# Kernel optimization log

Hardware: AMD Instinct MI355X
Metric: run time of the kernel (lower is better)

The kernel has to match this reference:

```python
import jax, jax.numpy as jnp
import numpy as np
from itertools import combinations

H_RANK_MAX = 2
TP_RANK_MAX = 2
BASIS_RANK_MAX = 2
DIM = 3
N_NODES = 50000
N_EDGES = 400000
N_CHANNELS = 16
R_CUT = 10.0  # radial cutoff for Bessel RBF (assumed)


def find_combinations(a_max, b_max, s):
    if s > a_max + b_max or s < 0:
        return []
    return [(a, s - a) for a in range(max(0, s - b_max), min(a_max, s) + 1)]


def contraction_is_valid(n_in, n_out):
    # legs are removed in pairs (Kronecker-delta contractions)
    return (n_in >= n_out) and ((n_in - n_out) % 2 == 0)


def _matchings(legs):
    # all perfect matchings of an even-size list of leg indices
    if not legs:
        yield []
        return
    a = legs[0]
    for i in range(1, len(legs)):
        rest = legs[1:i] + legs[i + 1:]
        for m in _matchings(rest):
            yield [(a, legs[i])] + m


def contraction_specs(a, b, c_out):
    # all einsum strings contracting an [E,K,dim^a] x [E,K,dim^b] tensor product
    # (a+b legs total) down to c_out free Cartesian legs, pairing the rest.
    n = a + b
    specs = []
    for free in combinations(range(n), c_out):
        paired = [i for i in range(n) if i not in free]
        for m in _matchings(paired):
            lbl = {}
            it = iter('mnopqrstuvwxyz')
            for f in free:
                lbl[f] = next(it)
            for (i, j) in m:
                L = next(it)
                lbl[i] = L
                lbl[j] = L
            sa = ''.join(lbl[i] for i in range(a))
            sb = ''.join(lbl[i] for i in range(a, n))
            so = ''.join(lbl[f] for f in free)
            specs.append(f'ek{sa},ek{sb}->ek{so}')
    return specs


def e_rbf(r, n):
    # Bessel radial basis: n is [K,1], r is [E] -> [K,E]
    return jnp.sqrt(2.0 / R_CUT) * jnp.sin(n * jnp.pi * r / R_CUT) / r


def tensor_prod(r, order):
    # repeated outer product of unit vectors: order 0 -> [E], order k -> [E] + [DIM]*k
    out = jnp.ones(r.shape[0], dtype=r.dtype)
    for _ in range(order):
        out = jnp.einsum('e...,ed->e...d', out, r)
    return out


def setup_inputs() -> dict:
    key = jax.random.key(0)
    ks = jax.random.split(key, 7)
    h0 = jax.random.normal(ks[0], (N_NODES, N_CHANNELS), jnp.float32)
    h1 = jax.random.normal(ks[1], (N_NODES, N_CHANNELS, DIM), jnp.float32)
    h2 = jax.random.normal(ks[2], (N_NODES, N_CHANNELS, DIM, DIM), jnp.float32)
    pos = jax.random.normal(ks[3], (N_NODES, DIM), jnp.float32)
    channel_weights = jax.random.normal(ks[4], (H_RANK_MAX + 1, N_CHANNELS, N_CHANNELS), jnp.float32)
    src = jax.random.randint(ks[5], (N_EDGES,), 0, N_NODES, dtype=jnp.int32)
    off = jax.random.randint(ks[6], (N_EDGES,), 1, N_NODES, dtype=jnp.int32)
    dst = (src + off) % N_NODES  # no self-loops -> no zero distances
    edge_index = jnp.stack([src, dst])
    return {"h0": h0, "h1": h1, "h2": h2, "pos": pos,
            "channel_weights": channel_weights, "edge_index": edge_index}


def reference(h0, h1, h2, pos, channel_weights, edge_index):
    h = [h0, h1, h2]
    src, dst = edge_index[0], edge_index[1]
    rel = pos[src] - pos[dst]                       # [E,3]
    dists = jnp.linalg.norm(rel, axis=-1)           # [E]
    unit = rel / dists[:, None]
    hg = [g[dst] for g in h]                        # per-edge gathered features
    # NOTE: the original forward computes channel-mixed self.h with channel_weights
    # but the contraction loop uses the UNMIXED gathered h (h[split[0]]); replicated here,
    # so channel_weights does not affect the output (zero gradient).
    n_vals = jnp.arange(1, N_CHANNELS + 1, dtype=dists.dtype)[:, None]  # [K,1]
    radial = e_rbf(dists, n_vals).reshape(N_EDGES, N_CHANNELS)  # faithful reshape (not transpose), as in source
    r_raw = [tensor_prod(unit, o) for o in range(TP_RANK_MAX + 1)]
    r_w = [jnp.einsum('ek,e...->ek...', radial, t) for t in r_raw]  # [E,K]+[3]*b
    outs = [None] * (BASIS_RANK_MAX + 1)
    for n_ind in range(H_RANK_MAX + TP_RANK_MAX + 1):
        for (a, b) in find_combinations(H_RANK_MAX, TP_RANK_MAX, n_ind):
            for br in range(BASIS_RANK_MAX + 1):
                if contraction_is_valid(n_ind, br):
                    for spec in contraction_specs(a, b, br):
                        t = jnp.einsum(spec, hg[a], r_w[b])
                        outs[br] = t if outs[br] is None else outs[br] + t
    # sum over paths (done incrementally above == stack + 'i...->...'), scatter to nodes
    res = []
    for t in outs:
        if t is not None:
            res.append(jax.ops.segment_sum(t, src, num_segments=N_NODES))
    return tuple(res)
```

## Files before the change

### kernel.cpp

```cpp
#include <hip/hip_runtime.h>
#include <hip/hip_fp16.h>
#include <math.h>

#define N_NODES   50000
#define N_EDGES   400000
#define NCH       16
#define CAP       48
#define EBUF_PAD  16
#define NSTRIPE   8
#define TPB       256
#define NBN       ((N_NODES + TPB - 1) / TPB)
#define NB_EDGES  ((N_EDGES + TPB - 1) / TPB)
#define NB_PACK   ((N_NODES * NCH + TPB - 1) / TPB)


__global__ void pack_kernel(const float* __restrict__ h0,
                            const float* __restrict__ h1,
                            const float* __restrict__ h2,
                            float4* __restrict__ hpack) {
    int nk = blockIdx.x * TPB + threadIdx.x;
    if (nk >= N_NODES * NCH) return;
    union { __half h[16]; float4 f[2]; } u;
    u.h[0] = __float2half(h0[nk]);
    const float* p1 = h1 + (size_t)nk * 3;
    u.h[1] = __float2half(p1[0]);
    u.h[2] = __float2half(p1[1]);
    u.h[3] = __float2half(p1[2]);
    const float* p2 = h2 + (size_t)nk * 9;
#pragma unroll
    for (int q = 0; q < 9; ++q) u.h[4 + q] = __float2half(p2[q]);
    u.h[13] = __half(0.0f);
    u.h[14] = __half(0.0f);
    u.h[15] = __half(0.0f);
    float4* o = hpack + (size_t)nk * 2;
    o[0] = u.f[0];
    o[1] = u.f[1];
}

__global__ void build_kernel(const float* __restrict__ pos,
                             const int* __restrict__ src,
                             const int* __restrict__ dst,
                             float* __restrict__ dists,
                             int* __restrict__ cnt,
                             int2* __restrict__ ebuf) {
    int e = blockIdx.x * TPB + threadIdx.x;
    if (e >= N_EDGES) return;
    int s = src[e];
    int d = dst[e];
    float rx = pos[3 * s + 0] - pos[3 * d + 0];
    float ry = pos[3 * s + 1] - pos[3 * d + 1];
    float rz = pos[3 * s + 2] - pos[3 * d + 2];
    float dist = sqrtf(rx * rx + ry * ry + rz * rz);
    dists[e] = dist;
    int slot = atomicAdd(&cnt[s], 1);
    if (slot < CAP) {
        ebuf[s * CAP + slot] = make_int2(e, d);
    }
}

__device__ __forceinline__ void edge_math(
    float ux, float uy, float uz, float R,
    float A0, const float A1[3], const float A2[9],
    float& acc0, float acc1[3], float acc2[9])
{
    float u[3] = {ux, uy, uz};
    float d1 = A1[0] * ux + A1[1] * uy + A1[2] * uz;
    float tA = A2[0] + A2[4] + A2[8];
    float v0 = A2[0] * ux + A2[1] * uy + A2[2] * uz;
    float v1 = A2[3] * ux + A2[4] * uy + A2[5] * uz;
    float v2 = A2[6] * ux + A2[7] * uy + A2[8] * uz;
    float w0 = A2[0] * ux + A2[3] * uy + A2[6] * uz;
    float w1 = A2[1] * ux + A2[4] * uy + A2[7] * uz;
    float w2 = A2[2] * ux + A2[5] * uy + A2[8] * uz;
    float q = ux * v0 + uy * v1 + uz * v2;

    acc0 += R * (2.0f * A0 + d1 + 2.0f * tA + 2.0f * q);

    float svw[3] = {v0 + w0, v1 + w1, v2 + w2};
    float a0t = A0 + tA;
#pragma unroll
    for (int mm = 0; mm < 3; ++mm) {
        acc1[mm] += R * (A0 * u[mm] + 2.0f * A1[mm] + 2.0f * d1 * u[mm]
                         + svw[mm] + tA * u[mm]);
#pragma unroll
        for (int nn = 0; nn < 3; ++nn) {
            acc2[3 * mm + nn] += R * (a0t * u[mm] * u[nn] + A1[mm] * u[nn]
                                      + 2.0f * A2[3 * mm + nn]
                                      + 2.0f * svw[mm] * u[nn]);
        }
    }
}

__device__ __forceinline__ void load_hset(
    const float* __restrict__ h0, const float* __restrict__ h1,
    const float* __restrict__ h2, const float* __restrict__ dists,
    int d, int e, int k,
    float& A0, float A1[3], float A2[9], float& r, float& nf)
{
    A0 = h0[d * NCH + k];
    const float* p1 = h1 + ((size_t)d * NCH + k) * 3;
    A1[0] = p1[0]; A1[1] = p1[1]; A1[2] = p1[2];
    const float* p2 = h2 + ((size_t)d * NCH + k) * 9;
#pragma unroll
    for (int q2 = 0; q2 < 9; ++q2) A2[q2] = p2[q2];
    unsigned f = (unsigned)e * NCH + (unsigned)k;
    unsigned n_idx = f / (unsigned)N_EDGES;
    unsigned e_idx = f - n_idx * (unsigned)N_EDGES;
    r = dists[e_idx];
    nf = (float)(n_idx + 1);
}

__device__ __forceinline__ float radial_R(float nf, float r) {
    return 0.44721359549995794f * __sinf(nf * 0.3141592653589793f * r) / r;
}

__global__ void node_wave_fast(const float4* __restrict__ hp,
                               const float* __restrict__ pos,
                               const int* __restrict__ cnt,
                               const int2* __restrict__ ebuf,
                               const float* __restrict__ dists,
                               float* __restrict__ out0,
                               float* __restrict__ out1,
                               float* __restrict__ out2) {
    int gid = blockIdx.x * TPB + threadIdx.x;
    int node = gid >> 6;
    if (node >= N_NODES) return;
    int lane = threadIdx.x & 63;
    int k = lane & 15;
    int j = lane >> 4;
    int base = node * CAP;

    int m = cnt[node];
    int2 pk = ebuf[base + j];
    float ps0 = pos[3 * node + 0];
    float ps1 = pos[3 * node + 1];
    float ps2 = pos[3 * node + 2];
    if (m > CAP) m = CAP;

    float acc0 = 0.0f;
    float acc1[3] = {0.0f, 0.0f, 0.0f};
    float acc2[9] = {0.0f, 0.0f, 0.0f, 0.0f, 0.0f, 0.0f, 0.0f, 0.0f, 0.0f};

    int c = j;
    while (c < m) {
        int cn = c + 4;
        int2 pkn = ebuf[base + cn];

        int e = pk.x;
        int d = pk.y;

        size_t hb = ((size_t)((d << 4) | k)) * 2;
        union { float4 f[2]; __half h[16]; } u;
        u.f[0] = hp[hb + 0];
        u.f[1] = hp[hb + 1];

        float pd0 = pos[3 * d + 0];
        float pd1 = pos[3 * d + 1];
        float pd2 = pos[3 * d + 2];

        unsigned f = (unsigned)e * NCH + (unsigned)k;
        unsigned n_idx = f / (unsigned)N_EDGES;
        unsigned e_idx = f - n_idx * (unsigned)N_EDGES;
        float r = dists[e_idx];
        float R = 0.44721359549995794f *
                  __sinf((float)(n_idx + 1) * 0.3141592653589793f * r) *
                  __builtin_amdgcn_rcpf(r);

        float rx = ps0 - pd0;
        float ry = ps1 - pd1;
        float rz = ps2 - pd2;
        float s2 = rx * rx + ry * ry + rz * rz;
        float inv = __builtin_amdgcn_rsqf(s2);

        float A0 = __half2float(u.h[0]);
        float A1[3] = {__half2float(u.h[1]), __half2float(u.h[2]),
                       __half2float(u.h[3])};
        float A2[9];
#pragma unroll
        for (int q2 = 0; q2 < 9; ++q2) A2[q2] = __half2float(u.h[4 + q2]);

        edge_math(rx * inv, ry * inv, rz * inv, R, A0, A1, A2,
                  acc0, acc1, acc2);

        pk = pkn;
        c = cn;
    }

    acc0 += __shfl_xor(acc0, 16, 64);
    acc0 += __shfl_xor(acc0, 32, 64);
#pragma unroll
    for (int mm = 0; mm < 3; ++mm) {
        acc1[mm] += __shfl_xor(acc1[mm], 16, 64);
        acc1[mm] += __shfl_xor(acc1[mm], 32, 64);
    }
#pragma unroll
    for (int mm = 0; mm < 9; ++mm) {
        acc2[mm] += __shfl_xor(acc2[mm], 16, 64);
        acc2[mm] += __shfl_xor(acc2[mm], 32, 64);
    }

    if (j == 0) {
        int t = node * NCH + k;
        out0[t] = acc0;
        float* o1p = out1 + (size_t)t * 3;
#pragma unroll
        for (int mm = 0; mm < 3; ++mm) o1p[mm] = acc1[mm];
        float* o2p = out2 + (size_t)t * 9;
#pragma unroll
        for (int mm = 0; mm < 9; ++mm) o2p[mm] = acc2[mm];
    }
}

__global__ void node_wave_mid(const float* __restrict__ h0,
                              const float* __restrict__ h1,
                              const float* __restrict__ h2,
                              const float* __restrict__ pos,
                              const int* __restrict__ cnt,
                              const int2* __restrict__ ebuf,
                              const float* __restrict__ dists,
                              float* __restrict__ out0,
                              float* __restrict__ out1,
                              float* __restrict__ out2) {
    int gid = blockIdx.x * TPB + threadIdx.x;
    int node = gid >> 6;
    if (node >= N_NODES) return;
    int lane = threadIdx.x & 63;
    int k = lane & 15;
    int j = lane >> 4;
    int base = node * CAP;

    int m = cnt[node];
    int2 pk = ebuf[base + j];
    float ps0 = pos[3 * node + 0];
    float ps1 = pos[3 * node + 1];
    float ps2 = pos[3 * node + 2];
    if (m > CAP) m = CAP;

    float acc0 = 0.0f;
    float acc1[3] = {0.0f, 0.0f, 0.0f};
    float acc2[9] = {0.0f, 0.0f, 0.0f, 0.0f, 0.0f, 0.0f, 0.0f, 0.0f, 0.0f};

    int c = j;
    while (c < m) {
        int cn = c + 4;
        int2 pkn = pk;
        if (cn < m) pkn = ebuf[base + cn];

        int e = pk.x;
        int d = pk.y;

        float pd0 = pos[3 * d + 0];
        float pd1 = pos[3 * d + 1];
        float pd2 = pos[3 * d + 2];

        float A0 = h0[d * NCH + k];
        const float* a1p = h1 + ((size_t)d * NCH + k) * 3;
        float A1[3] = {a1p[0], a1p[1], a1p[2]};
        const float* a2p = h2 + ((size_t)d * NCH + k) * 9;
        float A2[9];
#pragma unroll
        for (int q2 = 0; q2 < 9; ++q2) A2[q2] = a2p[q2];

        unsigned f = (unsigned)e * NCH + (unsigned)k;
        unsigned n_idx = f / (unsigned)N_EDGES;
        unsigned e_idx = f - n_idx * (unsigned)N_EDGES;
        float r = dists[e_idx];
        float R = 0.44721359549995794f *
                  __sinf((float)(n_idx + 1) * 0.3141592653589793f * r) / r;

        float rx = ps0 - pd0;
        float ry = ps1 - pd1;
        float rz = ps2 - pd2;
        float dist = sqrtf(rx * rx + ry * ry + rz * rz);
        float inv = 1.0f / dist;

        edge_math(rx * inv, ry * inv, rz * inv, R, A0, A1, A2, acc0, acc1, acc2);

        pk = pkn;
        c = cn;
    }

    acc0 += __shfl_xor(acc0, 16, 64);
    acc0 += __shfl_xor(acc0, 32, 64);
#pragma unroll
    for (int mm = 0; mm < 3; ++mm) {
        acc1[mm] += __shfl_xor(acc1[mm], 16, 64);
        acc1[mm] += __shfl_xor(acc1[mm], 32, 64);
    }
#pragma unroll
    for (int mm = 0; mm < 9; ++mm) {
        acc2[mm] += __shfl_xor(acc2[mm], 16, 64);
        acc2[mm] += __shfl_xor(acc2[mm], 32, 64);
    }

    if (j == 0) {
        int t = node * NCH + k;
        out0[t] = acc0;
        float* o1p = out1 + (size_t)t * 3;
#pragma unroll
        for (int mm = 0; mm < 3; ++mm) o1p[mm] = acc1[mm];
        float* o2p = out2 + (size_t)t * 9;
#pragma unroll
        for (int mm = 0; mm < 9; ++mm) o2p[mm] = acc2[mm];
    }
}


__global__ void fb_geom_hist(const float* __restrict__ pos,
                             const int* __restrict__ src,
                             const int* __restrict__ dst,
                             float* __restrict__ dists,
                             int* __restrict__ cnt8,
                             int* __restrict__ rankArr) {
    int e = blockIdx.x * TPB + threadIdx.x;
    if (e >= N_EDGES) return;
    int stripe = blockIdx.x & (NSTRIPE - 1);
    int s = src[e];
    int d = dst[e];
    float rx = pos[3 * s + 0] - pos[3 * d + 0];
    float ry = pos[3 * s + 1] - pos[3 * d + 1];
    float rz = pos[3 * s + 2] - pos[3 * d + 2];
    dists[e] = sqrtf(rx * rx + ry * ry + rz * rz);
    rankArr[e] = atomicAdd(&cnt8[stripe * N_NODES + s], 1);
}

__global__ void fb_scan(const int* __restrict__ cnt8,
                        int* __restrict__ incl,
                        int* __restrict__ bsum) {
    __shared__ int sh[TPB];
    int tid = threadIdx.x;
    int i = blockIdx.x * TPB + tid;
    int tot = 0;
    if (i < N_NODES) {
#pragma unroll
        for (int c = 0; c < NSTRIPE; ++c) tot += cnt8[c * N_NODES + i];
    }
    sh[tid] = tot;
    __syncthreads();
    for (int s = 1; s < TPB; s <<= 1) {
        int x = 0;
        if (tid >= s) x = sh[tid - s];
        __syncthreads();
        if (tid >= s) sh[tid] += x;
        __syncthreads();
    }
    if (i < N_NODES) incl[i] = sh[tid];
    if (tid == TPB - 1) bsum[blockIdx.x] = sh[TPB - 1];
}

__global__ void fb_final(const int* __restrict__ cnt8,
                         const int* __restrict__ incl,
                         const int* __restrict__ bsum,
                         int* __restrict__ offsets,
                         int* __restrict__ copyBase) {
    __shared__ int sh[TPB];
    int tid = threadIdx.x;
    int b = blockIdx.x;
    sh[tid] = (tid < b) ? bsum[tid] : 0;
    __syncthreads();
    for (int s = 128; s > 0; s >>= 1) {
        if (tid < s) sh[tid] += sh[tid + s];
        __syncthreads();
    }
    int base = sh[0];
    int i = b * TPB + tid;
    if (i < N_NODES) {
        int cv[NSTRIPE];
        int tot = 0;
#pragma unroll
        for (int c = 0; c < NSTRIPE; ++c) { cv[c] = cnt8[c * N_NODES + i]; tot += cv[c]; }
        int off = base + incl[i] - tot;
        offsets[i] = off;
        int run = off;
#pragma unroll
        for (int c = 0; c < NSTRIPE; ++c) { copyBase[c * N_NODES + i] = run; run += cv[c]; }
    }
    if (b == 0 && tid == 0) offsets[N_NODES] = N_EDGES;
}

__global__ void fb_fill(const int* __restrict__ src,
                        const int* __restrict__ dst,
                        const float* __restrict__ pos,
                        const float* __restrict__ dists,
                        const int* __restrict__ copyBase,
                        const int* __restrict__ rankArr,
                        float4* __restrict__ edata,
                        int* __restrict__ csr) {
    int e = blockIdx.x * TPB + threadIdx.x;
    if (e >= N_EDGES) return;
    int stripe = blockIdx.x & (NSTRIPE - 1);
    int s = src[e];
    int d = dst[e];
    float rx = pos[3 * s + 0] - pos[3 * d + 0];
    float ry = pos[3 * s + 1] - pos[3 * d + 1];
    float rz = pos[3 * s + 2] - pos[3 * d + 2];
    float inv = 1.0f / dists[e];
    int slot = copyBase[stripe * N_NODES + s] + rankArr[e];
    float4 ed;
    ed.x = rx * inv;
    ed.y = ry * inv;
    ed.z = rz * inv;
    ed.w = __int_as_float(d);
    edata[slot] = ed;
    csr[slot] = e;
}

__global__ void fb_main(const float* __restrict__ h0,
                        const float* __restrict__ h1,
                        const float* __restrict__ h2,
                        const int* __restrict__ offsets,
                        const float4* __restrict__ edata,
                        const int* __restrict__ csr,
                        const float* __restrict__ dists,
                        float* __restrict__ out0,
                        float* __restrict__ out1,
                        float* __restrict__ out2) {
    int gid = blockIdx.x * TPB + threadIdx.x;
    int node = gid >> 6;
    if (node >= N_NODES) return;
    int lane = threadIdx.x & 63;
    int k = lane & 15;
    int j = lane >> 4;
    int beg = offsets[node];
    int end = offsets[node + 1];

    float acc0 = 0.0f;
    float acc1[3] = {0.0f, 0.0f, 0.0f};
    float acc2[9] = {0.0f, 0.0f, 0.0f, 0.0f, 0.0f, 0.0f, 0.0f, 0.0f, 0.0f};

    int i = beg + j;
    float4 ed;
    int e = 0;
    if (i < end) { ed = edata[i]; e = csr[i]; }
    while (i < end) {
        int inext = i + 4;
        float4 edn = ed;
        int en = e;
        if (inext < end) { edn = edata[inext]; en = csr[inext]; }

        int d = __float_as_int(ed.w);
        float a0, a1[3], a2[9], r, nf;
        load_hset(h0, h1, h2, dists, d, e, k, a0, a1, a2, r, nf);
        float R = radial_R(nf, r);
        edge_math(ed.x, ed.y, ed.z, R, a0, a1, a2, acc0, acc1, acc2);

        ed = edn;
        e = en;
        i = inext;
    }

    acc0 += __shfl_xor(acc0, 16, 64);
    acc0 += __shfl_xor(acc0, 32, 64);
#pragma unroll
    for (int mm = 0; mm < 3; ++mm) {
        acc1[mm] += __shfl_xor(acc1[mm], 16, 64);
        acc1[mm] += __shfl_xor(acc1[mm], 32, 64);
    }
#pragma unroll
    for (int mm = 0; mm < 9; ++mm) {
        acc2[mm] += __shfl_xor(acc2[mm], 16, 64);
        acc2[mm] += __shfl_xor(acc2[mm], 32, 64);
    }

    if (j == 0) {
        int t = node * NCH + k;
        out0[t] = acc0;
        float* o1p = out1 + (size_t)t * 3;
#pragma unroll
        for (int mm = 0; mm < 3; ++mm) o1p[mm] = acc1[mm];
        float* o2p = out2 + (size_t)t * 9;
#pragma unroll
        for (int mm = 0; mm < 9; ++mm) o2p[mm] = acc2[mm];
    }
}


extern "C" void kernel_launch(void* const* d_in, const int* in_sizes, int n_in,
                              void* d_out, int out_size, void* d_ws, size_t ws_size,
                              hipStream_t stream) {
    const float* h0  = (const float*)d_in[0];
    const float* h1  = (const float*)d_in[1];
    const float* h2  = (const float*)d_in[2];
    const float* pos = (const float*)d_in[3];
    const int* edge_index = (const int*)d_in[5];
    const int* src = edge_index;
    const int* dst = edge_index + N_EDGES;

    float* out = (float*)d_out;
    float* out0 = out;
    float* out1 = out + (size_t)N_NODES * NCH;
    float* out2 = out + (size_t)N_NODES * NCH * 4;

    const size_t hpack_f4 = (size_t)N_NODES * NCH * 2;
    const size_t ebuf_n   = (size_t)N_NODES * CAP + EBUF_PAD;

    size_t needA = hpack_f4 * 16 + ebuf_n * 8
                 + (size_t)N_EDGES * 4 + (size_t)N_NODES * 4;
    size_t needB = ebuf_n * 8 + (size_t)N_EDGES * 4 + (size_t)N_NODES * 4;

    if (ws_size >= needA) {
        float4* hpack = (float4*)d_ws;
        int2* ebuf    = (int2*)(hpack + hpack_f4);
        float* dists  = (float*)(ebuf + ebuf_n);
        int* cnt      = (int*)(dists + N_EDGES);

        hipMemsetAsync(cnt, 0, N_NODES * sizeof(int), stream);
        pack_kernel<<<NB_PACK, TPB, 0, stream>>>(h0, h1, h2, hpack);
        build_kernel<<<NB_EDGES, TPB, 0, stream>>>(pos, src, dst, dists, cnt, ebuf);
        node_wave_fast<<<(N_NODES * 64 + TPB - 1) / TPB, TPB, 0, stream>>>(
            hpack, pos, cnt, ebuf, dists, out0, out1, out2);
    } else if (ws_size >= needB) {
        int2* ebuf   = (int2*)d_ws;
        float* dists = (float*)(ebuf + ebuf_n);
        int* cnt     = (int*)(dists + N_EDGES);

        hipMemsetAsync(cnt, 0, N_NODES * sizeof(int), stream);
        build_kernel<<<NB_EDGES, TPB, 0, stream>>>(pos, src, dst, dists, cnt, ebuf);
        node_wave_mid<<<(N_NODES * 64 + TPB - 1) / TPB, TPB, 0, stream>>>(
            h0, h1, h2, pos, cnt, ebuf, dists, out0, out1, out2);
    } else {
        float4* edata   = (float4*)d_ws;
        float*  dists   = (float*)(edata + N_EDGES);
        int* cnt8       = (int*)(dists + N_EDGES);
        int* rankArr    = cnt8 + NSTRIPE * N_NODES;
        int* incl       = rankArr + N_EDGES;
        int* bsum       = incl + N_NODES;
        int* offsets    = bsum + 256;
        int* copyBase   = offsets + N_NODES + 1;
        int* csr        = copyBase + NSTRIPE * N_NODES;

        hipMemsetAsync(cnt8, 0, NSTRIPE * N_NODES * sizeof(int), stream);
        fb_geom_hist<<<NB_EDGES, TPB, 0, stream>>>(pos, src, dst, dists, cnt8, rankArr);
        fb_scan<<<NBN, TPB, 0, stream>>>(cnt8, incl, bsum);
        fb_final<<<NBN, TPB, 0, stream>>>(cnt8, incl, bsum, offsets, copyBase);
        fb_fill<<<NB_EDGES, TPB, 0, stream>>>(src, dst, pos, dists, copyBase, rankArr, edata, csr);
        fb_main<<<(N_NODES * 64 + TPB - 1) / TPB, TPB, 0, stream>>>(
            h0, h1, h2, offsets, edata, csr, dists, out0, out1, out2);
    }
}
```

Measured before the change: 173.1 us.

## Merge pack and build kernels into one launch and refactor per-edge FMA math

The separate h-packing and edge-build kernels become a single prep kernel that splits work by block index, which removes one launch and lets the two independent jobs share the GPU. Separately, the per-edge contraction arithmetic is regrouped into explicit fmaf chains with hoisted common factors to cut instruction count. The regrouping changes floating-point rounding order slightly.

```diff
diff --git a/kernel.cpp b/kernel.cpp
--- a/kernel.cpp
+++ b/kernel.cpp
@@ -12,29 +12,53 @@
 #define NBN       ((N_NODES + TPB - 1) / TPB)
 #define NB_EDGES  ((N_EDGES + TPB - 1) / TPB)
 #define NB_PACK   ((N_NODES * NCH + TPB - 1) / TPB)
-
-
-__global__ void pack_kernel(const float* __restrict__ h0,
+#define NB_PREP   (NB_PACK + NB_EDGES)
+
+
+__global__ void prep_kernel(const float* __restrict__ h0,
                             const float* __restrict__ h1,
                             const float* __restrict__ h2,
-                            float4* __restrict__ hpack) {
-    int nk = blockIdx.x * TPB + threadIdx.x;
-    if (nk >= N_NODES * NCH) return;
-    union { __half h[16]; float4 f[2]; } u;
-    u.h[0] = __float2half(h0[nk]);
-    const float* p1 = h1 + (size_t)nk * 3;
-    u.h[1] = __float2half(p1[0]);
-    u.h[2] = __float2half(p1[1]);
-    u.h[3] = __float2half(p1[2]);
-    const float* p2 = h2 + (size_t)nk * 9;
-#pragma unroll
-    for (int q = 0; q < 9; ++q) u.h[4 + q] = __float2half(p2[q]);
-    u.h[13] = __half(0.0f);
-    u.h[14] = __half(0.0f);
-    u.h[15] = __half(0.0f);
-    float4* o = hpack + (size_t)nk * 2;
-    o[0] = u.f[0];
-    o[1] = u.f[1];
+                            const float* __restrict__ pos,
+                            const int* __restrict__ src,
+                            const int* __restrict__ dst,
+                            float4* __restrict__ hpack,
+                            float* __restrict__ dists,
+                            int* __restrict__ cnt,
+                            int2* __restrict__ ebuf) {
+    int b = blockIdx.x;
+    if (b < NB_PACK) {
+        int nk = b * TPB + threadIdx.x;
+        if (nk >= N_NODES * NCH) return;
+        union { __half h[16]; float4 f[2]; } u;
+        u.h[0] = __float2half(h0[nk]);
+        const float* p1 = h1 + (size_t)nk * 3;
+        u.h[1] = __float2half(p1[0]);
+        u.h[2] = __float2half(p1[1]);
+        u.h[3] = __float2half(p1[2]);
+        const float* p2 = h2 + (size_t)nk * 9;
+#pragma unroll
+        for (int q = 0; q < 9; ++q) u.h[4 + q] = __float2half(p2[q]);
+        u.h[13] = __half(0.0f);
+        u.h[14] = __half(0.0f);
+        u.h[15] = __half(0.0f);
+        float4* o = hpack + (size_t)nk * 2;
+        o[0] = u.f[0];
+        o[1] = u.f[1];
+    } else {
+        int e = (b - NB_PACK) * TPB + threadIdx.x;
+        if (e >= N_EDGES) return;
+        int s = src[e];
+        int d = dst[e];
+        float rx = pos[3 * s + 0] - pos[3 * d + 0];
+        float ry = pos[3 * s + 1] - pos[3 * d + 1];
+        float rz = pos[3 * s + 2] - pos[3 * d + 2];
+        float dist = sqrtf(rx * rx + ry * ry + rz * rz);
+        dists[e] = dist;
+        int slot = atomicAdd(&cnt[s], 1);
+        if (slot < CAP) {
+            ebuf[s * CAP + slot] = make_int2(e, d);
+        }
+    }
 }
 
 __global__ void build_kernel(const float* __restrict__ pos,
@@ -77,16 +101,25 @@
     acc0 += R * (2.0f * A0 + d1 + 2.0f * tA + 2.0f * q);
 
     float svw[3] = {v0 + w0, v1 + w1, v2 + w2};
+    float R2 = R + R;
     float a0t = A0 + tA;
+    float Rc1 = R * (a0t + 2.0f * d1);
 #pragma unroll
     for (int mm = 0; mm < 3; ++mm) {
-        acc1[mm] += R * (A0 * u[mm] + 2.0f * A1[mm] + 2.0f * d1 * u[mm]
-                         + svw[mm] + tA * u[mm]);
+        acc1[mm] = fmaf(Rc1, u[mm], acc1[mm]);
+        acc1[mm] = fmaf(R2, A1[mm], acc1[mm]);
+        acc1[mm] = fmaf(R, svw[mm], acc1[mm]);
+    }
+#pragma unroll
+    for (int mm = 0; mm < 3; ++mm) {
+        float t1 = fmaf(2.0f, svw[mm], A1[mm]);
+        float g = R * fmaf(a0t, u[mm], t1);
 #pragma unroll
         for (int nn = 0; nn < 3; ++nn) {
-            acc2[3 * mm + nn] += R * (a0t * u[mm] * u[nn] + A1[mm] * u[nn]
-                                      + 2.0f * A2[3 * mm + nn]
-                                      + 2.0f * svw[mm] * u[nn]);
+            float a = acc2[3 * mm + nn];
+            a = fmaf(g, u[nn], a);
+            a = fmaf(R2, A2[3 * mm + nn], a);
+            acc2[3 * mm + nn] = a;
         }
     }
 }
@@ -505,8 +538,8 @@
         int* cnt      = (int*)(dists + N_EDGES);
 
         hipMemsetAsync(cnt, 0, N_NODES * sizeof(int), stream);
-        pack_kernel<<<NB_PACK, TPB, 0, stream>>>(h0, h1, h2, hpack);
-        build_kernel<<<NB_EDGES, TPB, 0, stream>>>(pos, src, dst, dists, cnt, ebuf);
+        prep_kernel<<<NB_PREP, TPB, 0, stream>>>(h0, h1, h2, pos, src, dst,
+                                                 hpack, dists, cnt, ebuf);
         node_wave_fast<<<(N_NODES * 64 + TPB - 1) / TPB, TPB, 0, stream>>>(
             hpack, pos, cnt, ebuf, dists, out0, out1, out2);
     } else if (ws_size >= needB) {
```

New measurement: 168.5 us, median of 2. 1.03x faster.
